# Performance work log

Hardware: AMD Instinct MI355X
Metric: run time of the kernel (lower is better)

Reference implementation:

```python
import jax, jax.numpy as jnp
import numpy as np


def setup_inputs() -> dict:
    key = jax.random.key(0)
    k1, k2, k3, k4 = jax.random.split(key, 4)
    B, H, S, D = 2, 16, 2048, 64
    q = jax.random.normal(k1, (B, H, S, D), dtype=jnp.float32)
    k = jax.random.normal(k2, (B, H, S, D), dtype=jnp.float32)
    v = jax.random.normal(k3, (B, H, S, D), dtype=jnp.float32)
    mask = jax.random.randint(k4, (1, 1, S, S), 0, 2, dtype=jnp.int32)
    return {"q": q, "k": k, "v": v, "mask": mask}


def reference(q, k, v, mask):
    # scores: [B,H,S,S] -- intentionally materialized as in the original
    d = k.shape[-1]
    scale = 1.0 / jnp.sqrt(jnp.asarray(d, dtype=q.dtype))
    x = jnp.einsum("bhqd,bhkd->bhqk", q, k) * scale
    x = x + mask.astype(x.dtype) * jnp.asarray(-10000.0, dtype=x.dtype)
    p = jax.nn.softmax(x, axis=-1)  # dropout is identity in eval mode
    return jnp.einsum("bhqk,bhkd->bhqd", p, v)
```

## Files before the change

kernel.cpp:

```cpp
#include <hip/hip_runtime.h>


#define S_LEN 2048
#define D_DIM 64
#define N_KT 32
#define NBH 32
#define TILE_SEGS 16
#define TILE_SHORTS 8192
#define SEG_U32 256

typedef __attribute__((ext_vector_type(8))) short bf16x8;
typedef __attribute__((ext_vector_type(16))) float f32x16;
typedef __attribute__((ext_vector_type(2))) __fp16 fp16x2;
typedef unsigned int u32;

#define C1 0.180336880111121f
#define CM (-14426.9504088896f)

static __device__ __forceinline__ unsigned short f2bf(float f) {
  union { float f; unsigned u; } x; x.f = f;
  return (unsigned short)((x.u + 0x8000u) >> 16);
}
static __device__ __forceinline__ unsigned packbf(float lo, float hi) {
  union { float f; unsigned u; } a, b; a.f = lo; b.f = hi;
  return ((a.u + 0x8000u) >> 16) | ((b.u + 0x8000u) & 0xffff0000u);
}
static __device__ __forceinline__ f32x16 zero16() {
  f32x16 z;
#pragma unroll
  for (int i = 0; i < 16; ++i) z[i] = 0.f;
  return z;
}
static __device__ __forceinline__ void dma16(const u32* g, u32* l) {
  __builtin_amdgcn_global_load_lds(
      (const __attribute__((address_space(1))) u32*)g,
      (__attribute__((address_space(3))) u32*)l, 16, 0, 0);
}
static __device__ __forceinline__ unsigned pkh(float lo, float hi) {
  union { fp16x2 h; unsigned u; } x;
  x.h = __builtin_amdgcn_cvt_pkrtz(lo, hi);
  return x.u;
}

__global__ __launch_bounds__(256) void prep_fused(
    const float* __restrict__ k, const float* __restrict__ v,
    const int* __restrict__ mask, unsigned short* __restrict__ kvws,
    u32* __restrict__ mw) {
  __shared__ unsigned short Kr[64 * 72];
  __shared__ unsigned short Vr[64 * 72];
  const int blk = blockIdx.x;
  const int t = threadIdx.x;
  if (blk < N_KT * NBH) {
    const int kt = blk & 31, bh = blk >> 5;
    const size_t goff = (size_t)bh * (S_LEN * D_DIM) + (size_t)kt * 64 * D_DIM;
    const float4* kg = (const float4*)(k + goff);
    const float4* vg = (const float4*)(v + goff);
#pragma unroll
    for (int j = 0; j < 4; ++j) {
      const int i = t + j * 256;
      const int row = i >> 4, c4 = i & 15;
      const float4 x = kg[i];
      ushort4 w;
      w.x = f2bf(x.x); w.y = f2bf(x.y); w.z = f2bf(x.z); w.w = f2bf(x.w);
      *(ushort4*)&Kr[row * 72 + c4 * 4] = w;
      const float4 y = vg[i];
      const unsigned p01 = pkh(y.x, y.y), p23 = pkh(y.z, y.w);
      uint2 vv; vv.x = p01; vv.y = p23;
      *(uint2*)&Vr[row * 72 + c4 * 4] = vv;
    }
    __syncthreads();
    uint4* img = (uint4*)(kvws + (size_t)(bh * N_KT + kt) * TILE_SHORTS);
    for (int c = t; c < 512; c += 256) {
      const int col = c & 31, hlc = (c >> 5) & 1, ks = (c >> 6) & 3, khc = c >> 8;
      img[c] = *(const uint4*)&Kr[(khc * 32 + col) * 72 + ks * 16 + hlc * 8];
    }
    for (int c = t; c < 512; c += 256) {
      const int col = c & 31, b = (c >> 5) & 1, hlc = (c >> 6) & 1, kcHi = c >> 7;
      const int d = b * 32 + col, kk = (2 * kcHi + hlc) * 8;
      union { unsigned short s[8]; uint4 u; } o;
#pragma unroll
      for (int jj = 0; jj < 8; ++jj) o.s[jj] = Vr[(kk + jj) * 72 + d];
      img[512 + c] = o.u;
    }
  } else {
    const int gt = (blk - N_KT * NBH) * 256 + t;
    const int q4 = gt & 3;
    const int kt = (gt >> 2) & 31;
    const int hl = (gt >> 7) & 1;
    const int row = gt >> 8;
    const int j0 = kt * 64 + 32 * (q4 >> 1) + 16 * (q4 & 1) + 4 * hl;
    const int* mr = mask + (size_t)row * S_LEN;
    const int4 a = *(const int4*)(mr + j0);
    const int4 b = *(const int4*)(mr + j0 + 8);
    uint4 w;
    w.x = (a.x == 0 ? 0x0000FFFFu : 0u) | (a.y == 0 ? 0xFFFF0000u : 0u);
    w.y = (a.z == 0 ? 0x0000FFFFu : 0u) | (a.w == 0 ? 0xFFFF0000u : 0u);
    w.z = (b.x == 0 ? 0x0000FFFFu : 0u) | (b.y == 0 ? 0xFFFF0000u : 0u);
    w.w = (b.z == 0 ? 0x0000FFFFu : 0u) | (b.w == 0 ? 0xFFFF0000u : 0u);
    *(uint4*)&mw[((size_t)(row * 2 + hl) * N_KT + kt) * 16 + q4 * 4] = w;
  }
}

__global__ __launch_bounds__(256, 4) void attn_fwd(
    const float* __restrict__ q, const unsigned short* __restrict__ kvws,
    const u32* __restrict__ mw, float* __restrict__ out) {
  const int qt = blockIdx.x;
  const int bh = blockIdx.y;
  const size_t hoff = (size_t)bh * (S_LEN * D_DIM);

  __shared__ unsigned short sbuf[2][TILE_SHORTS];

  const int t = threadIdx.x;
  const int wave = t >> 6;
  const int lane = t & 63;
  const int col = lane & 31;
  const int hl = lane >> 5;
  const int qh = wave >> 1;
  const int kh = wave & 1;
  const int qg = qt * 64 + qh * 32 + col;

  bf16x8 bQ[4];
  {
    const float* qrow = q + hoff + (size_t)qg * D_DIM;
#pragma unroll
    for (int ks = 0; ks < 4; ++ks) {
      const float4 x0 = *(const float4*)(qrow + ks * 16 + hl * 8);
      const float4 x1 = *(const float4*)(qrow + ks * 16 + hl * 8 + 4);
      union { bf16x8 v; unsigned d[4]; } u;
      u.d[0] = packbf(x0.x * C1, x0.y * C1);
      u.d[1] = packbf(x0.z * C1, x0.w * C1);
      u.d[2] = packbf(x1.x * C1, x1.y * C1);
      u.d[3] = packbf(x1.z * C1, x1.w * C1);
      bQ[ks] = u.v;
    }
  }

  f32x16 oT0 = zero16(), oT1 = zero16();
  float lacc0 = 0.f, lacc1 = 0.f;
  const uint4* mrow = (const uint4*)(mw + (size_t)(qg * 2 + hl) * N_KT * 16);
  const u32* img = (const u32*)(kvws + (size_t)bh * N_KT * TILE_SHORTS);
  const int seg0 = wave * 4;

#if __has_builtin(__builtin_amdgcn_fdot2)
  const fp16x2 ones2 = {(__fp16)1.0f, (__fp16)1.0f};
#endif

  uint4 mq0, mq1;
  {
    const uint4* mp = mrow + kh * 2;
    asm volatile("global_load_dwordx4 %0, %2, off\n\t"
                 "global_load_dwordx4 %1, %3, off"
                 : "=&v"(mq0), "=&v"(mq1)
                 : "v"(mp), "v"(mp + 1)
                 : "memory");
  }
#pragma unroll
  for (int s = 0; s < 4; ++s)
    dma16(img + (size_t)(seg0 + s) * SEG_U32 + lane * 4,
          (u32*)&sbuf[0][0] + (seg0 + s) * SEG_U32);
#pragma unroll
  for (int s = 0; s < 4; ++s)
    dma16(img + (size_t)(TILE_SEGS + seg0 + s) * SEG_U32 + lane * 4,
          (u32*)&sbuf[1][0] + (seg0 + s) * SEG_U32);

  for (int kt = 0; kt < N_KT; ++kt) {
    const int p = kt & 1;
    if (kt < N_KT - 1) {
      asm volatile("s_waitcnt vmcnt(4)" ::: "memory");
    } else {
      asm volatile("s_waitcnt vmcnt(0)" ::: "memory");
    }
    __builtin_amdgcn_s_barrier();
    __builtin_amdgcn_sched_barrier(0);

    const unsigned short* Ksb = &sbuf[p][0];
    const unsigned short* Vtb = &sbuf[p][4096];
    const u32 mwv[8] = {mq0.x, mq0.y, mq0.z, mq0.w,
                        mq1.x, mq1.y, mq1.z, mq1.w};

    f32x16 sT = zero16();
#pragma unroll
    for (int ks = 0; ks < 4; ++ks) {
      const bf16x8 aK =
          *(const bf16x8*)&Ksb[kh * 2048 + ks * 512 + hl * 256 + col * 8];
      sT = __builtin_amdgcn_mfma_f32_32x32x16_bf16(aK, bQ[ks], sT, 0, 0, 0);
    }

    unsigned pw[8];
#pragma unroll
    for (int g2 = 0; g2 < 4; ++g2) {
      const float e0 = __builtin_amdgcn_exp2f(sT[g2 * 4 + 0]);
      const float e1 = __builtin_amdgcn_exp2f(sT[g2 * 4 + 1]);
      const float e2 = __builtin_amdgcn_exp2f(sT[g2 * 4 + 2]);
      const float e3 = __builtin_amdgcn_exp2f(sT[g2 * 4 + 3]);
#if __has_builtin(__builtin_amdgcn_fdot2)
      const unsigned w0 = pkh(e0, e1) & mwv[g2 * 2 + 0];
      const unsigned w1 = pkh(e2, e3) & mwv[g2 * 2 + 1];
      pw[g2 * 2 + 0] = w0;
      pw[g2 * 2 + 1] = w1;
      union { unsigned u; fp16x2 h; } c0, c1;
      c0.u = w0; c1.u = w1;
      lacc0 = __builtin_amdgcn_fdot2(c0.h, ones2, lacc0, false);
      lacc1 = __builtin_amdgcn_fdot2(c1.h, ones2, lacc1, false);
#else
      const u32 mlo = mwv[g2 * 2 + 0], mhi = mwv[g2 * 2 + 1];
      const float e0m = (mlo & 0xFFFFu) ? e0 : 0.f;
      const float e1m = (mlo >> 16) ? e1 : 0.f;
      const float e2m = (mhi & 0xFFFFu) ? e2 : 0.f;
      const float e3m = (mhi >> 16) ? e3 : 0.f;
      pw[g2 * 2 + 0] = pkh(e0m, e1m);
      pw[g2 * 2 + 1] = pkh(e2m, e3m);
      lacc0 += e0m + e1m;
      lacc1 += e2m + e3m;
#endif
    }

#pragma unroll
    for (int ks2 = 0; ks2 < 2; ++ks2) {
      const unsigned d0 = pw[4 * ks2 + 0], d1 = pw[4 * ks2 + 1];
      const unsigned d2 = pw[4 * ks2 + 2], d3 = pw[4 * ks2 + 3];
      const unsigned s0 = hl ? d0 : d2;
      const unsigned s1 = hl ? d1 : d3;
      const unsigned r0 = (unsigned)__shfl_xor((int)s0, 32);
      const unsigned r1 = (unsigned)__shfl_xor((int)s1, 32);
      union { bf16x8 v; unsigned d[4]; } pf;
      pf.d[0] = hl ? r0 : d0;
      pf.d[1] = hl ? r1 : d1;
      pf.d[2] = hl ? d2 : r0;
      pf.d[3] = hl ? d3 : r1;
      const int kcHi = kh * 2 + ks2;
      const bf16x8 aV0 =
          *(const bf16x8*)&Vtb[kcHi * 1024 + hl * 512 + 0 * 256 + col * 8];
      const bf16x8 aV1 =
          *(const bf16x8*)&Vtb[kcHi * 1024 + hl * 512 + 1 * 256 + col * 8];
      oT0 = __builtin_amdgcn_mfma_f32_32x32x16_f16(aV0, pf.v, oT0, 0, 0, 0);
      oT1 = __builtin_amdgcn_mfma_f32_32x32x16_f16(aV1, pf.v, oT1, 0, 0, 0);
    }

    if (kt < N_KT - 1) {
      asm volatile("s_waitcnt lgkmcnt(0)" ::: "memory");
      __builtin_amdgcn_s_barrier();
      __builtin_amdgcn_sched_barrier(0);
      {
        const uint4* mp = mrow + (kt + 1) * 4 + kh * 2;
        asm volatile("global_load_dwordx4 %0, %2, off\n\t"
                     "global_load_dwordx4 %1, %3, off"
                     : "=&v"(mq0), "=&v"(mq1)
                     : "v"(mp), "v"(mp + 1)
                     : "memory");
      }
      if (kt < N_KT - 2) {
        const u32* g = img + (size_t)(kt + 2) * (TILE_SEGS * SEG_U32);
#pragma unroll
        for (int s = 0; s < 4; ++s)
          dma16(g + (size_t)(seg0 + s) * SEG_U32 + lane * 4,
                (u32*)&sbuf[p][0] + (seg0 + s) * SEG_U32);
      }
    }
  }

  __syncthreads();
  {
    float* xb = (float*)&sbuf[0][0];
    float* lb = (float*)((char*)&sbuf[0][0] + 17408);
    const float lsum = lacc0 + lacc1;
    const float l2 = lsum + __shfl_xor(lsum, 32);
    float* xr = xb + (size_t)(qh * 32 + col) * 68;
    if (kh) {
#pragma unroll
      for (int rg = 0; rg < 4; ++rg) {
        float4 w0, w1;
        w0.x = oT0[rg * 4 + 0]; w0.y = oT0[rg * 4 + 1];
        w0.z = oT0[rg * 4 + 2]; w0.w = oT0[rg * 4 + 3];
        w1.x = oT1[rg * 4 + 0]; w1.y = oT1[rg * 4 + 1];
        w1.z = oT1[rg * 4 + 2]; w1.w = oT1[rg * 4 + 3];
        *(float4*)(xr + 8 * rg + 4 * hl) = w0;
        *(float4*)(xr + 32 + 8 * rg + 4 * hl) = w1;
      }
      if (!hl) lb[qh * 32 + col] = l2;
    }
    __syncthreads();
    if (!kh) {
      const float inv = 1.0f / (l2 + lb[qh * 32 + col]);
      float* orow = out + hoff + (size_t)qg * D_DIM;
#pragma unroll
      for (int rg = 0; rg < 4; ++rg) {
        const float4 a0 = *(const float4*)(xr + 8 * rg + 4 * hl);
        const float4 a1 = *(const float4*)(xr + 32 + 8 * rg + 4 * hl);
        float4 w0, w1;
        w0.x = (oT0[rg * 4 + 0] + a0.x) * inv;
        w0.y = (oT0[rg * 4 + 1] + a0.y) * inv;
        w0.z = (oT0[rg * 4 + 2] + a0.z) * inv;
        w0.w = (oT0[rg * 4 + 3] + a0.w) * inv;
        w1.x = (oT1[rg * 4 + 0] + a1.x) * inv;
        w1.y = (oT1[rg * 4 + 1] + a1.y) * inv;
        w1.z = (oT1[rg * 4 + 2] + a1.z) * inv;
        w1.w = (oT1[rg * 4 + 3] + a1.w) * inv;
        *(float4*)(orow + 8 * rg + 4 * hl) = w0;
        *(float4*)(orow + 32 + 8 * rg + 4 * hl) = w1;
      }
    }
  }
}

#define LDK 72
#define LDV 72
__global__ __launch_bounds__(256, 2) void attn_fwd_self(
    const float* __restrict__ q, const float* __restrict__ k,
    const float* __restrict__ v, const int* __restrict__ mask,
    float* __restrict__ out) {
  const int qt = blockIdx.x;
  const int bh = blockIdx.y;
  const size_t hoff = (size_t)bh * (S_LEN * D_DIM);
  __shared__ unsigned short Ks[64 * LDK];
  __shared__ unsigned short Vt[64 * LDV];
  const int t = threadIdx.x;
  const int wave = t >> 6;
  const int lane = t & 63;
  const int col = lane & 31;
  const int hl = lane >> 5;
  const int sw = col >> 2;
  const int qg = qt * 128 + wave * 32 + col;
  bf16x8 bQ[4];
  {
    const float* qrow = q + hoff + (size_t)qg * D_DIM;
#pragma unroll
    for (int ks = 0; ks < 4; ++ks) {
      const float4 x0 = *(const float4*)(qrow + ks * 16 + hl * 8);
      const float4 x1 = *(const float4*)(qrow + ks * 16 + hl * 8 + 4);
      union { bf16x8 v; unsigned d[4]; } u;
      u.d[0] = packbf(x0.x, x0.y);
      u.d[1] = packbf(x0.z, x0.w);
      u.d[2] = packbf(x1.x, x1.y);
      u.d[3] = packbf(x1.z, x1.w);
      bQ[ks] = u.v;
    }
  }
  float4 pk[4], pv[4];
  {
    const float4* kg = (const float4*)(k + hoff);
    const float4* vg = (const float4*)(v + hoff);
#pragma unroll
    for (int j = 0; j < 4; ++j) { pk[j] = kg[t + j * 256]; pv[j] = vg[t + j * 256]; }
  }
  f32x16 oT0 = zero16(), oT1 = zero16();
  float lacc = 0.f;
  const int* mrow = mask + (size_t)qg * S_LEN;
  for (int kt = 0; kt < N_KT; ++kt) {
    __syncthreads();
#pragma unroll
    for (int j = 0; j < 4; ++j) {
      const int i = t + j * 256;
      const int row = i >> 4, c4 = i & 15;
      ushort4 w;
      w.x = f2bf(pk[j].x); w.y = f2bf(pk[j].y);
      w.z = f2bf(pk[j].z); w.w = f2bf(pk[j].w);
      *(ushort4*)&Ks[row * LDK + c4 * 4] = w;
      const int swc = 8 * (((row >> 3) + c4) & 7) + (row & 7);
      Vt[(4 * c4 + 0) * LDV + swc] = f2bf(pv[j].x);
      Vt[(4 * c4 + 1) * LDV + swc] = f2bf(pv[j].y);
      Vt[(4 * c4 + 2) * LDV + swc] = f2bf(pv[j].z);
      Vt[(4 * c4 + 3) * LDV + swc] = f2bf(pv[j].w);
    }
    __syncthreads();
    if (kt + 1 < N_KT) {
      const float4* kg = (const float4*)(k + hoff + (size_t)(kt + 1) * 64 * D_DIM);
      const float4* vg = (const float4*)(v + hoff + (size_t)(kt + 1) * 64 * D_DIM);
#pragma unroll
      for (int j = 0; j < 4; ++j) { pk[j] = kg[t + j * 256]; pv[j] = vg[t + j * 256]; }
    }
    int4 mq[2][4];
#pragma unroll
    for (int kb = 0; kb < 2; ++kb)
#pragma unroll
      for (int g = 0; g < 4; ++g)
        mq[kb][g] = *(const int4*)(mrow + kt * 64 + kb * 32 + g * 8 + hl * 4);
    f32x16 sT0 = zero16(), sT1 = zero16();
#pragma unroll
    for (int ks = 0; ks < 4; ++ks) {
      const bf16x8 aK0 = *(const bf16x8*)&Ks[col * LDK + ks * 16 + hl * 8];
      const bf16x8 aK1 = *(const bf16x8*)&Ks[(32 + col) * LDK + ks * 16 + hl * 8];
      sT0 = __builtin_amdgcn_mfma_f32_32x32x16_bf16(aK0, bQ[ks], sT0, 0, 0, 0);
      sT1 = __builtin_amdgcn_mfma_f32_32x32x16_bf16(aK1, bQ[ks], sT1, 0, 0, 0);
    }
    unsigned pw[2][8];
#pragma unroll
    for (int kb = 0; kb < 2; ++kb) {
      const f32x16 sT = kb ? sT1 : sT0;
      float e[16];
#pragma unroll
      for (int g = 0; g < 4; ++g) {
        const int4 mv = mq[kb][g];
        const int* mvp = &mv.x;
#pragma unroll
        for (int r3 = 0; r3 < 4; ++r3) {
          const int reg = g * 4 + r3;
          const float bias = mvp[r3] ? CM : 0.0f;
          const float ev = __builtin_amdgcn_exp2f(fmaf(sT[reg], C1, bias));
          e[reg] = ev;
          lacc += ev;
        }
        pw[kb][g * 2 + 0] = packbf(e[g * 4 + 0], e[g * 4 + 1]);
        pw[kb][g * 2 + 1] = packbf(e[g * 4 + 2], e[g * 4 + 3]);
      }
    }
#pragma unroll
    for (int ks = 0; ks < 4; ++ks) {
      const int kb = ks >> 1, h = ks & 1;
      const unsigned d0 = pw[kb][4 * h + 0], d1 = pw[kb][4 * h + 1];
      const unsigned d2 = pw[kb][4 * h + 2], d3 = pw[kb][4 * h + 3];
      const unsigned s0 = hl ? d0 : d2;
      const unsigned s1 = hl ? d1 : d3;
      const unsigned r0 = (unsigned)__shfl_xor((int)s0, 32);
      const unsigned r1 = (unsigned)__shfl_xor((int)s1, 32);
      union { bf16x8 v; unsigned d[4]; } pf;
      pf.d[0] = hl ? r0 : d0;
      pf.d[1] = hl ? r1 : d1;
      pf.d[2] = hl ? d2 : r0;
      pf.d[3] = hl ? d3 : r1;
      const int cpr = 8 * (((2 * ks + hl) + sw) & 7);
      const bf16x8 aV0 = *(const bf16x8*)&Vt[col * LDV + cpr];
      const bf16x8 aV1 = *(const bf16x8*)&Vt[(32 + col) * LDV + cpr];
      oT0 = __builtin_amdgcn_mfma_f32_32x32x16_bf16(aV0, pf.v, oT0, 0, 0, 0);
      oT1 = __builtin_amdgcn_mfma_f32_32x32x16_bf16(aV1, pf.v, oT1, 0, 0, 0);
    }
  }
  const float ltot = lacc + __shfl_xor(lacc, 32);
  const float inv = 1.0f / ltot;
  float* orow = out + hoff + (size_t)qg * D_DIM;
#pragma unroll
  for (int rg = 0; rg < 4; ++rg) {
    float4 w0, w1;
    w0.x = oT0[rg * 4 + 0] * inv; w0.y = oT0[rg * 4 + 1] * inv;
    w0.z = oT0[rg * 4 + 2] * inv; w0.w = oT0[rg * 4 + 3] * inv;
    w1.x = oT1[rg * 4 + 0] * inv; w1.y = oT1[rg * 4 + 1] * inv;
    w1.z = oT1[rg * 4 + 2] * inv; w1.w = oT1[rg * 4 + 3] * inv;
    *(float4*)(orow + 8 * rg + 4 * hl) = w0;
    *(float4*)(orow + 32 + 8 * rg + 4 * hl) = w1;
  }
}

extern "C" void kernel_launch(void* const* d_in, const int* in_sizes, int n_in,
                              void* d_out, int out_size, void* d_ws, size_t ws_size,
                              hipStream_t stream) {
  const float* q = (const float*)d_in[0];
  const float* k = (const float*)d_in[1];
  const float* v = (const float*)d_in[2];
  const int* mask = (const int*)d_in[3];
  float* out = (float*)d_out;

  const size_t kv_shorts = (size_t)NBH * N_KT * TILE_SHORTS;
  const size_t mw_words = (size_t)S_LEN * 2 * N_KT * 16;
  const size_t need = kv_shorts * sizeof(unsigned short) + mw_words * 4;

  if (ws_size >= need) {
    unsigned short* kvws = (unsigned short*)d_ws;
    u32* mwp = (u32*)(kvws + kv_shorts);
    prep_fused<<<dim3(N_KT * NBH + (S_LEN * 2 * N_KT * 4) / 256), dim3(256), 0,
                 stream>>>(k, v, mask, kvws, mwp);
    attn_fwd<<<dim3(S_LEN / 64, NBH), dim3(256), 0, stream>>>(q, kvws, mwp, out);
  } else {
    attn_fwd_self<<<dim3(S_LEN / 128, NBH), dim3(256), 0, stream>>>(q, k, v, mask, out);
  }
}
```

Measured before the change: 163.9 us.

## Compute softmax row sums via MFMA, add setprio and XCD-aware block mapping

Replaces the per-lane fdot2 accumulation of softmax denominators with an extra MFMA that multiplies a ones matrix by the probability fragment, moving that reduction onto the matrix core. It also wraps the MFMA sections in s_setprio to favour matrix issue across waves. Block indices are remapped so that the four heads assigned to an XCD share its L2 for the K/V images. The extra MFMA adds matrix-core work on every tile, and the remap only helps if blocks really are dispatched round-robin across XCDs.

Measured after the change: 167.0 us. About the same (+1.9%).

```diff
diff --git a/kernel.cpp b/kernel.cpp
--- a/kernel.cpp
+++ b/kernel.cpp
@@ -104,8 +104,11 @@
 __global__ __launch_bounds__(256, 4) void attn_fwd(
     const float* __restrict__ q, const unsigned short* __restrict__ kvws,
     const u32* __restrict__ mw, float* __restrict__ out) {
-  const int qt = blockIdx.x;
-  const int bh = blockIdx.y;
+  const int lin = blockIdx.x + 32 * blockIdx.y;
+  const int xcd = lin & 7;
+  const int wk = lin >> 3;
+  const int qt = wk & 31;
+  const int bh = xcd * 4 + (wk >> 5);
   const size_t hoff = (size_t)bh * (S_LEN * D_DIM);
 
   __shared__ unsigned short sbuf[2][TILE_SHORTS];
@@ -135,15 +138,17 @@
     }
   }
 
-  f32x16 oT0 = zero16(), oT1 = zero16();
-  float lacc0 = 0.f, lacc1 = 0.f;
+  bf16x8 onesA;
+  {
+    union { bf16x8 v; unsigned d[4]; } u;
+    u.d[0] = u.d[1] = u.d[2] = u.d[3] = 0x3C003C00u;
+    onesA = u.v;
+  }
+
+  f32x16 oT0 = zero16(), oT1 = zero16(), oL = zero16();
   const uint4* mrow = (const uint4*)(mw + (size_t)(qg * 2 + hl) * N_KT * 16);
   const u32* img = (const u32*)(kvws + (size_t)bh * N_KT * TILE_SHORTS);
   const int seg0 = wave * 4;
-
-#if __has_builtin(__builtin_amdgcn_fdot2)
-  const fp16x2 ones2 = {(__fp16)1.0f, (__fp16)1.0f};
-#endif
 
   uint4 mq0, mq1;
   {
@@ -179,12 +184,14 @@
                         mq1.x, mq1.y, mq1.z, mq1.w};
 
     f32x16 sT = zero16();
+    __builtin_amdgcn_s_setprio(1);
 #pragma unroll
     for (int ks = 0; ks < 4; ++ks) {
       const bf16x8 aK =
           *(const bf16x8*)&Ksb[kh * 2048 + ks * 512 + hl * 256 + col * 8];
       sT = __builtin_amdgcn_mfma_f32_32x32x16_bf16(aK, bQ[ks], sT, 0, 0, 0);
     }
+    __builtin_amdgcn_s_setprio(0);
 
     unsigned pw[8];
 #pragma unroll
@@ -193,28 +200,11 @@
       const float e1 = __builtin_amdgcn_exp2f(sT[g2 * 4 + 1]);
       const float e2 = __builtin_amdgcn_exp2f(sT[g2 * 4 + 2]);
       const float e3 = __builtin_amdgcn_exp2f(sT[g2 * 4 + 3]);
-#if __has_builtin(__builtin_amdgcn_fdot2)
-      const unsigned w0 = pkh(e0, e1) & mwv[g2 * 2 + 0];
-      const unsigned w1 = pkh(e2, e3) & mwv[g2 * 2 + 1];
-      pw[g2 * 2 + 0] = w0;
-      pw[g2 * 2 + 1] = w1;
-      union { unsigned u; fp16x2 h; } c0, c1;
-      c0.u = w0; c1.u = w1;
-      lacc0 = __builtin_amdgcn_fdot2(c0.h, ones2, lacc0, false);
-      lacc1 = __builtin_amdgcn_fdot2(c1.h, ones2, lacc1, false);
-#else
-      const u32 mlo = mwv[g2 * 2 + 0], mhi = mwv[g2 * 2 + 1];
-      const float e0m = (mlo & 0xFFFFu) ? e0 : 0.f;
-      const float e1m = (mlo >> 16) ? e1 : 0.f;
-      const float e2m = (mhi & 0xFFFFu) ? e2 : 0.f;
-      const float e3m = (mhi >> 16) ? e3 : 0.f;
-      pw[g2 * 2 + 0] = pkh(e0m, e1m);
-      pw[g2 * 2 + 1] = pkh(e2m, e3m);
-      lacc0 += e0m + e1m;
-      lacc1 += e2m + e3m;
-#endif
-    }
-
+      pw[g2 * 2 + 0] = pkh(e0, e1) & mwv[g2 * 2 + 0];
+      pw[g2 * 2 + 1] = pkh(e2, e3) & mwv[g2 * 2 + 1];
+    }
+
+    __builtin_amdgcn_s_setprio(1);
 #pragma unroll
     for (int ks2 = 0; ks2 < 2; ++ks2) {
       const unsigned d0 = pw[4 * ks2 + 0], d1 = pw[4 * ks2 + 1];
@@ -235,7 +225,9 @@
           *(const bf16x8*)&Vtb[kcHi * 1024 + hl * 512 + 1 * 256 + col * 8];
       oT0 = __builtin_amdgcn_mfma_f32_32x32x16_f16(aV0, pf.v, oT0, 0, 0, 0);
       oT1 = __builtin_amdgcn_mfma_f32_32x32x16_f16(aV1, pf.v, oT1, 0, 0, 0);
-    }
+      oL = __builtin_amdgcn_mfma_f32_32x32x16_f16(onesA, pf.v, oL, 0, 0, 0);
+    }
+    __builtin_amdgcn_s_setprio(0);
 
     if (kt < N_KT - 1) {
       asm volatile("s_waitcnt lgkmcnt(0)" ::: "memory");
@@ -263,8 +255,6 @@
   {
     float* xb = (float*)&sbuf[0][0];
     float* lb = (float*)((char*)&sbuf[0][0] + 17408);
-    const float lsum = lacc0 + lacc1;
-    const float l2 = lsum + __shfl_xor(lsum, 32);
     float* xr = xb + (size_t)(qh * 32 + col) * 68;
     if (kh) {
 #pragma unroll
@@ -277,11 +267,11 @@
         *(float4*)(xr + 8 * rg + 4 * hl) = w0;
         *(float4*)(xr + 32 + 8 * rg + 4 * hl) = w1;
       }
-      if (!hl) lb[qh * 32 + col] = l2;
+      if (!hl) lb[qh * 32 + col] = oL[0];
     }
     __syncthreads();
     if (!kh) {
-      const float inv = 1.0f / (l2 + lb[qh * 32 + col]);
+      const float inv = 1.0f / (oL[0] + lb[qh * 32 + col]);
       float* orow = out + hoff + (size_t)qg * D_DIM;
 #pragma unroll
       for (int rg = 0; rg < 4; ++rg) {
```
